# Kernel optimization log

Measured on AMD Instinct MI355X. Metric: run time of the kernel, lower is better.

## Reference

```python
import jax, jax.numpy as jnp
import numpy as np

B, L, D = 4, 4096, 64

def setup_inputs() -> dict:
    key = jax.random.key(0)
    k1, k2, k3, k4 = jax.random.split(key, 4)
    return {
        "query": jax.random.normal(k1, (B, L, D), dtype=jnp.float32),
        "key": jax.random.normal(k2, (B, L, D), dtype=jnp.float32),
        "value": jax.random.normal(k3, (B, L, D), dtype=jnp.float32),
        "mask": jax.random.uniform(k4, (B, L, L), dtype=jnp.float32),
        "d_k": D,
    }

def reference(query, key, value, mask, d_k):
    # scores: [B, Lq, Lk] = Q @ K^T / sqrt(d_k), then multiplicative mask
    scale = 1.0 / jnp.sqrt(jnp.asarray(d_k, dtype=query.dtype))
    scores = jnp.einsum("bqd,bkd->bqk", query, key) * scale * mask
    attn = jax.nn.softmax(scores, axis=-1)  # row-wise over keys
    return jnp.einsum("bqk,bkd->bqd", attn, value)
```

## Files before the change

kernel.cpp:

```cpp
#include <hip/hip_runtime.h>
#include <hip/hip_bf16.h>
#include <stdint.h>
#include <stddef.h>

#define B_   4
#define L_   4096
#define D_   64
#define TK_  64
#define NKT  (L_/TK_)
#define TQ_  64
#define NQB  (L_/TQ_)
#define KROW 144
#define TILE_BYTES (64*KROW)

typedef __attribute__((ext_vector_type(8))) short bf16x8;
typedef __attribute__((ext_vector_type(4))) float f32x4;
typedef __attribute__((ext_vector_type(4))) unsigned short u16x4;

__device__ static inline unsigned short f2bf(float x) {
  union { __hip_bfloat16 h; unsigned short u; } cv;
  cv.h = __float2bfloat16(x);
  return cv.u;
}

__device__ static inline void gl_lds16(const char* g, char* l) {
  __builtin_amdgcn_global_load_lds(
      (const __attribute__((address_space(1))) void*)g,
      (__attribute__((address_space(3))) void*)l, 16, 0, 0);
}

__global__ __launch_bounds__(256) void prep_kv(const float* __restrict__ K,
                                               const float* __restrict__ V,
                                               char* __restrict__ kws,
                                               char* __restrict__ vws) {
  const int blk = blockIdx.x;
  const int kt  = blk & (NKT-1);
  const int b   = blk >> 6;
  const int t   = threadIdx.x;
  const int kr  = t >> 2;
  const int ds  = t & 3;
  const size_t row = (size_t)b*L_ + (size_t)kt*TK_ + kr;
  const f32x4* kp = (const f32x4*)(K + row*D_ + ds*16);
  const f32x4* vp = (const f32x4*)(V + row*D_ + ds*16);
  f32x4 kv[4], vv[4];
  for (int s=0;s<4;++s){ kv[s]=kp[s]; vv[s]=vp[s]; }

  bf16x8 lo, hi;
  for (int s=0;s<2;++s) for (int j=0;j<4;++j) lo[s*4+j] = (short)f2bf(kv[s  ][j]);
  for (int s=0;s<2;++s) for (int j=0;j<4;++j) hi[s*4+j] = (short)f2bf(kv[2+s][j]);
  const int slot = (kr&3)*16 + (kr>>2);
  char* kdst = kws + (size_t)blk*TILE_BYTES + slot*KROW + ds*32;
  *(bf16x8*)(kdst)    = lo;
  *(bf16x8*)(kdst+16) = hi;

  char* vdst = vws + (size_t)blk*TILE_BYTES + kr*2;
  for (int s=0;s<4;++s)
    for (int j=0;j<4;++j)
      *(unsigned short*)(vdst + (size_t)(ds*16 + s*4 + j)*KROW) = f2bf(vv[s][j]);
}

__global__ __launch_bounds__(256) void attn_main(const float* __restrict__ Q,
                                                 const float* __restrict__ Mk,
                                                 const char* __restrict__ kws,
                                                 const char* __restrict__ vws,
                                                 float* __restrict__ out) {
  __shared__ char Kbuf[2][TILE_BYTES];
  __shared__ char Vbuf[2][TILE_BYTES];
  __shared__ char Pbuf[4][16*KROW];

  const int blk  = blockIdx.x;
  const int qt   = blk & (NQB-1);
  const int b    = blk >> 6;
  const int tid  = threadIdx.x;
  const int w    = tid >> 6;
  const int lane = tid & 63;
  const int i16  = lane & 15;
  const int quad = lane >> 4;
  const int q0   = qt*TQ_ + w*16;

  const float cs = 0.125f * 1.44269504088896f;
  bf16x8 aq[2];
  {
    const float* qp = Q + ((size_t)b*L_ + q0 + i16)*D_ + quad*8;
    for (int ks=0; ks<2; ++ks) {
      const f32x4* p = (const f32x4*)(qp + ks*32);
      f32x4 x0 = p[0], x1 = p[1];
      bf16x8 v;
      for (int j=0;j<4;++j) v[j]   = (short)f2bf(x0[j]*cs);
      for (int j=0;j<4;++j) v[4+j] = (short)f2bf(x1[j]*cs);
      aq[ks] = v;
    }
  }

  const float* mbase = Mk + ((size_t)b*L_ + q0 + quad*4)*(size_t)L_ + 4*i16;

  f32x4 O[4];
  for (int t=0;t<4;++t) O[t] = (f32x4){0.f,0.f,0.f,0.f};
  float l_acc[4] = {0.f,0.f,0.f,0.f};
  f32x4 cmv[4], nmv[4];

  const size_t tb0 = (size_t)(b*NKT)*TILE_BYTES;

  {
    const char* ks0 = kws + tb0;
    const char* vs0 = vws + tb0;
    for (int c=w; c<18; c+=4) {
      if (c<9) gl_lds16(ks0 + c*1024     + lane*16, &Kbuf[0][c*1024]);
      else     gl_lds16(vs0 + (c-9)*1024 + lane*16, &Vbuf[0][(c-9)*1024]);
    }
    for (int r=0;r<4;++r) cmv[r] = *(const f32x4*)(mbase + (size_t)r*L_);
  }
  __syncthreads();

  for (int kt=0; kt<NKT; ++kt) {
    const int buf = kt & 1;
    if (kt+1 < NKT) {
      const char* ksrc = kws + tb0 + (size_t)(kt+1)*TILE_BYTES;
      const char* vsrc = vws + tb0 + (size_t)(kt+1)*TILE_BYTES;
      for (int c=w; c<18; c+=4) {
        if (c<9) gl_lds16(ksrc + c*1024     + lane*16, &Kbuf[buf^1][c*1024]);
        else     gl_lds16(vsrc + (c-9)*1024 + lane*16, &Vbuf[buf^1][(c-9)*1024]);
      }
      const size_t kc = (size_t)(kt+1)*TK_;
      for (int r=0;r<4;++r) nmv[r] = *(const f32x4*)(mbase + (size_t)r*L_ + kc);
    }

    f32x4 acc[4];
    const char* kb = Kbuf[buf];
#pragma unroll
    for (int t=0;t<4;++t) {
      acc[t] = (f32x4){0.f,0.f,0.f,0.f};
#pragma unroll
      for (int ks=0;ks<2;++ks) {
        bf16x8 bf = *(const bf16x8*)(kb + (t*16+i16)*KROW + ks*64 + quad*16);
        acc[t] = __builtin_amdgcn_mfma_f32_16x16x32_bf16(aq[ks], bf, acc[t], 0,0,0);
      }
    }

    float p[16]; float rs[4] = {0.f,0.f,0.f,0.f};
#pragma unroll
    for (int t=0;t<4;++t)
#pragma unroll
      for (int r=0;r<4;++r) {
        float v = __builtin_amdgcn_exp2f(acc[t][r] * cmv[r][t]);
        p[t*4+r] = v; rs[r] += v;
      }
#pragma unroll
    for (int r=0;r<4;++r) {
      float s = rs[r];
      s += __shfl_xor(s, 1); s += __shfl_xor(s, 2);
      s += __shfl_xor(s, 4); s += __shfl_xor(s, 8);
      l_acc[r] += s;
    }

    char* pb = Pbuf[w];
#pragma unroll
    for (int r=0;r<4;++r) {
      u16x4 pk;
      for (int t=0;t<4;++t) pk[t] = f2bf(p[t*4+r]);
      *(u16x4*)(pb + (quad*4+r)*KROW + i16*8) = pk;
    }

    const char* vb = Vbuf[buf];
#pragma unroll
    for (int ks=0;ks<2;++ks) {
      bf16x8 af = *(const bf16x8*)(pb + i16*KROW + ks*64 + quad*16);
#pragma unroll
      for (int dt=0;dt<4;++dt) {
        bf16x8 vf = *(const bf16x8*)(vb + (dt*16+i16)*KROW + ks*64 + quad*16);
        O[dt] = __builtin_amdgcn_mfma_f32_16x16x32_bf16(af, vf, O[dt], 0,0,0);
      }
    }

    __syncthreads();
    if (kt+1 < NKT) for (int r=0;r<4;++r) cmv[r] = nmv[r];
  }

  float inv[4];
#pragma unroll
  for (int r=0;r<4;++r) inv[r] = 1.0f / l_acc[r];
#pragma unroll
  for (int t=0;t<4;++t)
#pragma unroll
    for (int r=0;r<4;++r)
      out[((size_t)b*L_ + q0 + quad*4 + r)*D_ + t*16 + i16] = O[t][r]*inv[r];
}

extern "C" void kernel_launch(void* const* d_in, const int* in_sizes, int n_in,
                              void* d_out, int out_size, void* d_ws, size_t ws_size,
                              hipStream_t stream) {
  const float* Q  = (const float*)d_in[0];
  const float* K  = (const float*)d_in[1];
  const float* V  = (const float*)d_in[2];
  const float* Mk = (const float*)d_in[3];

  char* kws = (char*)d_ws;
  char* vws = kws + (size_t)B_*NKT*TILE_BYTES;

  prep_kv  <<<B_*NKT, 256, 0, stream>>>(K, V, kws, vws);
  attn_main<<<B_*NQB, 256, 0, stream>>>(Q, Mk, kws, vws, (float*)d_out);
}
```

Baseline: 405.6 us.

## Fuse K/V bf16 conversion into attention kernel, drop prep pass

```diff
diff --git a/kernel.cpp b/kernel.cpp
--- a/kernel.cpp
+++ b/kernel.cpp
@@ -11,7 +11,6 @@
 #define TQ_  64
 #define NQB  (L_/TQ_)
 #define KROW 144
-#define TILE_BYTES (64*KROW)
 
 typedef __attribute__((ext_vector_type(8))) short bf16x8;
 typedef __attribute__((ext_vector_type(4))) float f32x4;
@@ -23,54 +22,18 @@
   return cv.u;
 }
 
-__device__ static inline void gl_lds16(const char* g, char* l) {
-  __builtin_amdgcn_global_load_lds(
-      (const __attribute__((address_space(1))) void*)g,
-      (__attribute__((address_space(3))) void*)l, 16, 0, 0);
-}
-
-__global__ __launch_bounds__(256) void prep_kv(const float* __restrict__ K,
-                                               const float* __restrict__ V,
-                                               char* __restrict__ kws,
-                                               char* __restrict__ vws) {
-  const int blk = blockIdx.x;
-  const int kt  = blk & (NKT-1);
-  const int b   = blk >> 6;
-  const int t   = threadIdx.x;
-  const int kr  = t >> 2;
-  const int ds  = t & 3;
-  const size_t row = (size_t)b*L_ + (size_t)kt*TK_ + kr;
-  const f32x4* kp = (const f32x4*)(K + row*D_ + ds*16);
-  const f32x4* vp = (const f32x4*)(V + row*D_ + ds*16);
-  f32x4 kv[4], vv[4];
-  for (int s=0;s<4;++s){ kv[s]=kp[s]; vv[s]=vp[s]; }
-
-  bf16x8 lo, hi;
-  for (int s=0;s<2;++s) for (int j=0;j<4;++j) lo[s*4+j] = (short)f2bf(kv[s  ][j]);
-  for (int s=0;s<2;++s) for (int j=0;j<4;++j) hi[s*4+j] = (short)f2bf(kv[2+s][j]);
-  const int slot = (kr&3)*16 + (kr>>2);
-  char* kdst = kws + (size_t)blk*TILE_BYTES + slot*KROW + ds*32;
-  *(bf16x8*)(kdst)    = lo;
-  *(bf16x8*)(kdst+16) = hi;
-
-  char* vdst = vws + (size_t)blk*TILE_BYTES + kr*2;
-  for (int s=0;s<4;++s)
-    for (int j=0;j<4;++j)
-      *(unsigned short*)(vdst + (size_t)(ds*16 + s*4 + j)*KROW) = f2bf(vv[s][j]);
-}
-
-__global__ __launch_bounds__(256) void attn_main(const float* __restrict__ Q,
-                                                 const float* __restrict__ Mk,
-                                                 const char* __restrict__ kws,
-                                                 const char* __restrict__ vws,
-                                                 float* __restrict__ out) {
-  __shared__ char Kbuf[2][TILE_BYTES];
-  __shared__ char Vbuf[2][TILE_BYTES];
+__global__ __launch_bounds__(256) void attn_fused(
+    const float* __restrict__ Q, const float* __restrict__ K,
+    const float* __restrict__ V, const float* __restrict__ Mk,
+    float* __restrict__ out) {
+  __shared__ char Kbuf[2][TK_*KROW];
+  __shared__ char Vbuf[2][TK_*KROW];
   __shared__ char Pbuf[4][16*KROW];
 
-  const int blk  = blockIdx.x;
-  const int qt   = blk & (NQB-1);
-  const int b    = blk >> 6;
+  const int idx = blockIdx.x;
+  const int b   = (idx & 7) >> 1;
+  const int qt  = ((idx >> 3) << 1) | (idx & 1);
+
   const int tid  = threadIdx.x;
   const int w    = tid >> 6;
   const int lane = tid & 63;
@@ -78,10 +41,14 @@
   const int quad = lane >> 4;
   const int q0   = qt*TQ_ + w*16;
 
+  const int dq = tid & 15;
+  const int kq = tid >> 4;
+
   const float cs = 0.125f * 1.44269504088896f;
   bf16x8 aq[2];
   {
     const float* qp = Q + ((size_t)b*L_ + q0 + i16)*D_ + quad*8;
+#pragma unroll
     for (int ks=0; ks<2; ++ks) {
       const f32x4* p = (const f32x4*)(qp + ks*32);
       f32x4 x0 = p[0], x1 = p[1];
@@ -93,36 +60,54 @@
   }
 
   const float* mbase = Mk + ((size_t)b*L_ + q0 + quad*4)*(size_t)L_ + 4*i16;
+  const float* kbase = K + ((size_t)b*L_ + kq*4)*D_ + dq*4;
+  const float* vbase = V + ((size_t)b*L_ + kq*4)*D_ + dq*4;
 
   f32x4 O[4];
+#pragma unroll
   for (int t=0;t<4;++t) O[t] = (f32x4){0.f,0.f,0.f,0.f};
   float l_acc[4] = {0.f,0.f,0.f,0.f};
   f32x4 cmv[4], nmv[4];
+  f32x4 kreg[4], vreg[4];
 
-  const size_t tb0 = (size_t)(b*NKT)*TILE_BYTES;
-
-  {
-    const char* ks0 = kws + tb0;
-    const char* vs0 = vws + tb0;
-    for (int c=w; c<18; c+=4) {
-      if (c<9) gl_lds16(ks0 + c*1024     + lane*16, &Kbuf[0][c*1024]);
-      else     gl_lds16(vs0 + (c-9)*1024 + lane*16, &Vbuf[0][(c-9)*1024]);
-    }
-    for (int r=0;r<4;++r) cmv[r] = *(const f32x4*)(mbase + (size_t)r*L_);
+#pragma unroll
+  for (int r=0;r<4;++r) {
+    kreg[r] = *(const f32x4*)(kbase + (size_t)r*D_);
+    vreg[r] = *(const f32x4*)(vbase + (size_t)r*D_);
+    cmv[r]  = *(const f32x4*)(mbase + (size_t)r*L_);
   }
-  __syncthreads();
+#pragma unroll
+  for (int r=0;r<4;++r) nmv[r] = cmv[r];
 
   for (int kt=0; kt<NKT; ++kt) {
     const int buf = kt & 1;
+
+    {
+      char* kb = Kbuf[buf]; char* vb = Vbuf[buf];
+#pragma unroll
+      for (int r=0;r<4;++r) {
+        u16x4 pk;
+        for (int j=0;j<4;++j) pk[j] = f2bf(kreg[r][j]);
+        *(u16x4*)(kb + (r*16+kq)*KROW + dq*8) = pk;
+      }
+#pragma unroll
+      for (int e=0;e<4;++e) {
+        u16x4 pv;
+        for (int r=0;r<4;++r) pv[r] = f2bf(vreg[r][e]);
+        *(u16x4*)(vb + (dq*4+e)*KROW + kq*8) = pv;
+      }
+    }
+    __syncthreads();
+
     if (kt+1 < NKT) {
-      const char* ksrc = kws + tb0 + (size_t)(kt+1)*TILE_BYTES;
-      const char* vsrc = vws + tb0 + (size_t)(kt+1)*TILE_BYTES;
-      for (int c=w; c<18; c+=4) {
-        if (c<9) gl_lds16(ksrc + c*1024     + lane*16, &Kbuf[buf^1][c*1024]);
-        else     gl_lds16(vsrc + (c-9)*1024 + lane*16, &Vbuf[buf^1][(c-9)*1024]);
+      const size_t roff = (size_t)(kt+1)*TK_*(size_t)D_;
+      const size_t kc   = (size_t)(kt+1)*TK_;
+#pragma unroll
+      for (int r=0;r<4;++r) {
+        kreg[r] = *(const f32x4*)(kbase + roff + (size_t)r*D_);
+        vreg[r] = *(const f32x4*)(vbase + roff + (size_t)r*D_);
+        nmv[r]  = *(const f32x4*)(mbase + (size_t)r*L_ + kc);
       }
-      const size_t kc = (size_t)(kt+1)*TK_;
-      for (int r=0;r<4;++r) nmv[r] = *(const f32x4*)(mbase + (size_t)r*L_ + kc);
     }
 
     f32x4 acc[4];
@@ -132,8 +117,8 @@
       acc[t] = (f32x4){0.f,0.f,0.f,0.f};
 #pragma unroll
       for (int ks=0;ks<2;++ks) {
-        bf16x8 bf = *(const bf16x8*)(kb + (t*16+i16)*KROW + ks*64 + quad*16);
-        acc[t] = __builtin_amdgcn_mfma_f32_16x16x32_bf16(aq[ks], bf, acc[t], 0,0,0);
+        bf16x8 bfr = *(const bf16x8*)(kb + (t*16+i16)*KROW + ks*64 + quad*16);
+        acc[t] = __builtin_amdgcn_mfma_f32_16x16x32_bf16(aq[ks], bfr, acc[t], 0,0,0);
       }
     }
 
@@ -172,8 +157,8 @@
       }
     }
 
-    __syncthreads();
-    if (kt+1 < NKT) for (int r=0;r<4;++r) cmv[r] = nmv[r];
+#pragma unroll
+    for (int r=0;r<4;++r) cmv[r] = nmv[r];
   }
 
   float inv[4];
@@ -193,10 +178,7 @@
   const float* K  = (const float*)d_in[1];
   const float* V  = (const float*)d_in[2];
   const float* Mk = (const float*)d_in[3];
+  (void)d_ws; (void)ws_size;
 
-  char* kws = (char*)d_ws;
-  char* vws = kws + (size_t)B_*NKT*TILE_BYTES;
-
-  prep_kv  <<<B_*NKT, 256, 0, stream>>>(K, V, kws, vws);
-  attn_main<<<B_*NQB, 256, 0, stream>>>(Q, Mk, kws, vws, (float*)d_out);
+  attn_fused<<<B_*NQB, 256, 0, stream>>>(Q, K, V, Mk, (float*)d_out);
 }
```

Result: slower. 428.7 us (+5.7%).
